# Performance work log

Measured on AMD Instinct MI355X. Metric: run time of the kernel, lower is better.

## Reference

```python
import jax, jax.numpy as jnp
import numpy as np

E, H, I = 8, 1024, 512          # experts, hidden, moe_intermediate
NG, TKG, TOPK = 4, 2, 4          # n_group, topk_group, num_experts_per_tok
SCALE = 2.5                      # routed_scaling_factor


def _mlp(x, wg, wu, wd):
    # SwiGLU MLP: down(silu(gate(x)) * up(x)), all bias-free
    return (jax.nn.silu(x @ wg) * (x @ wu)) @ wd


def setup_inputs() -> dict:
    key = jax.random.key(0)
    ks = jax.random.split(key, 8)
    s = 0.02
    return {
        "hidden_states": jax.random.normal(ks[0], (32, 256, H), jnp.float32),
        "gate_w": jax.random.normal(ks[1], (E, H), jnp.float32) * np.float32(np.sqrt(2.0 / H)),
        "correction_bias": jnp.zeros((E,), jnp.float32),
        "Wg": jax.random.normal(ks[2], (E, H, I), jnp.float32) * s,
        "Wu": jax.random.normal(ks[3], (E, H, I), jnp.float32) * s,
        "Wd": jax.random.normal(ks[4], (E, I, H), jnp.float32) * s,
        "Wg_s": jax.random.normal(ks[5], (H, I), jnp.float32) * s,
        "Wu_s": jax.random.normal(ks[6], (H, I), jnp.float32) * s,
        "Wd_s": jax.random.normal(ks[7], (I, H), jnp.float32) * s,
    }


def reference(hidden_states, gate_w, correction_bias, Wg, Wu, Wd, Wg_s, Wu_s, Wd_s):
    B, T, _ = hidden_states.shape
    x = hidden_states.reshape(-1, H)                     # [N, H]
    N = x.shape[0]

    # ---- TopkRouter + route_tokens_to_experts (float32 router math) ----
    logits = x @ gate_w.T                                # [N, E]
    scores = jax.nn.sigmoid(logits)
    scores_c = scores + correction_bias                  # scores for choice
    grp = scores_c.reshape(N, NG, E // NG)
    group_scores = jnp.sum(jax.lax.top_k(grp, 2)[0], axis=-1)        # [N, NG]
    grp_idx = jax.lax.top_k(group_scores, TKG)[1]                    # [N, TKG]
    group_mask = jnp.zeros_like(group_scores).at[
        jnp.arange(N)[:, None], grp_idx].set(1.0)                    # [N, NG]
    score_mask = jnp.repeat(group_mask, E // NG, axis=-1) > 0.5      # [N, E]
    scores_for_choice = jnp.where(score_mask, scores_c, 0.0)
    topk_idx = jax.lax.top_k(scores_for_choice, TOPK)[1]             # [N, K]
    topk_w = jnp.take_along_axis(scores, topk_idx, axis=-1)          # [N, K]
    topk_w = topk_w / (jnp.sum(topk_w, axis=-1, keepdims=True) + 1e-20)
    topk_w = topk_w * SCALE

    # ---- DSNaiveMoE: equivalent dense-expert combine ----
    # combine weight per (token, expert); zero for unrouted pairs, so the
    # dense evaluation produces exactly the gather/scatter loop's result.
    cw = jnp.sum(jax.nn.one_hot(topk_idx, E, dtype=topk_w.dtype) * topk_w[..., None], axis=1)  # [N, E]
    g = jnp.einsum('nh,ehi->eni', x, Wg)
    u = jnp.einsum('nh,ehi->eni', x, Wu)
    y = jnp.einsum('eni,eih->enh', jax.nn.silu(g) * u, Wd)           # [E, N, H]
    routed = jnp.einsum('enh,ne->nh', y, cw)                          # [N, H]

    # ---- shared expert on residual input (replaces residual add) ----
    out = routed + _mlp(x, Wg_s, Wu_s, Wd_s)
    return out.reshape(B, T, H)
```

## Files before the change

kernel.cpp:

```cpp
#include <hip/hip_runtime.h>

#define E_ 8
#define H_ 1024
#define I_ 512
#define NE 9
#define NTOK 8192

typedef __bf16 bf16;
typedef __bf16 bf16x8 __attribute__((ext_vector_type(8)));
typedef __bf16 bf16x4 __attribute__((ext_vector_type(4)));
typedef float f32x4 __attribute__((ext_vector_type(4)));

__device__ __forceinline__ void gload16(const bf16* g, bf16* l) {
  __builtin_amdgcn_global_load_lds(
      (const __attribute__((address_space(1))) void*)g,
      (__attribute__((address_space(3))) void*)l,
      16, 0, 0);
}

__global__ __launch_bounds__(256) void convert_kernel(
    const float* __restrict__ x, bf16* __restrict__ xb) {
  int i = blockIdx.x * 256 + threadIdx.x;
  f32x4 v = ((const f32x4*)x)[i];
  bf16x4 o = {(bf16)v.x, (bf16)v.y, (bf16)v.z, (bf16)v.w};
  ((bf16x4*)xb)[i] = o;
}

__global__ __launch_bounds__(256) void router_kernel(
    const float* __restrict__ x, const float* __restrict__ gw,
    const float* __restrict__ bias, int4* __restrict__ topk_e,
    float4* __restrict__ topk_w) {
  int t = threadIdx.x;
  int l = t & 63, w = t >> 6;
  int n = blockIdx.x * 4 + w;
  const f32x4* xr = (const f32x4*)(x + (size_t)n * H_ + l * 16);
  float xv[16];
#pragma unroll
  for (int q = 0; q < 4; q++) {
    f32x4 v = xr[q];
    xv[q * 4 + 0] = v.x; xv[q * 4 + 1] = v.y; xv[q * 4 + 2] = v.z; xv[q * 4 + 3] = v.w;
  }
  float s[E_], sc[E_];
#pragma unroll
  for (int e = 0; e < E_; e++) {
    const f32x4* gr = (const f32x4*)(gw + e * H_ + l * 16);
    float acc = 0.f;
#pragma unroll
    for (int q = 0; q < 4; q++) {
      f32x4 g = gr[q];
      acc += xv[q * 4 + 0] * g.x + xv[q * 4 + 1] * g.y + xv[q * 4 + 2] * g.z + xv[q * 4 + 3] * g.w;
    }
#pragma unroll
    for (int off = 32; off > 0; off >>= 1) acc += __shfl_xor(acc, off, 64);
    float sig = 1.f / (1.f + __expf(-acc));
    s[e] = sig;
    sc[e] = sig + bias[e];
  }
  if (l == 0) {
    float gs[4];
#pragma unroll
    for (int g = 0; g < 4; g++) gs[g] = sc[2 * g] + sc[2 * g + 1];
    int g0 = 0;
    for (int g = 1; g < 4; g++) if (gs[g] > gs[g0]) g0 = g;
    int g1 = -1;
    for (int g = 0; g < 4; g++) {
      if (g == g0) continue;
      if (g1 < 0 || gs[g] > gs[g1]) g1 = g;
    }
    int es[4] = {2 * g0, 2 * g0 + 1, 2 * g1, 2 * g1 + 1};
    float wsum = 1e-20f;
    for (int j = 0; j < 4; j++) wsum += s[es[j]];
    float inv = 2.5f / wsum;
    topk_e[n] = (int4){es[0], es[1], es[2], es[3]};
    topk_w[n] = (float4){s[es[0]] * inv, s[es[1]] * inv, s[es[2]] * inv, s[es[3]] * inv};
  }
}

__global__ __launch_bounds__(256) void compact_kernel(
    const int4* __restrict__ topk_e, const float4* __restrict__ topk_w,
    int* __restrict__ cnt, int* __restrict__ idx, float* __restrict__ cwp,
    int* __restrict__ tokpos) {
  __shared__ int hist[E_];
  __shared__ int base[E_];
  int t = threadIdx.x;
  if (t < E_) hist[t] = 0;
  __syncthreads();
  int n = blockIdx.x * 256 + t;
  int4 e4 = topk_e[n];
  float4 w4 = topk_w[n];
  int le[4] = {e4.x, e4.y, e4.z, e4.w};
  float lw[4] = {w4.x, w4.y, w4.z, w4.w};
  int lpos[4];
#pragma unroll
  for (int j = 0; j < 4; j++) lpos[j] = atomicAdd(&hist[le[j]], 1);
  __syncthreads();
  if (t < E_) base[t] = atomicAdd(&cnt[t], hist[t]);
  __syncthreads();
#pragma unroll
  for (int j = 0; j < 4; j++) {
    int p = base[le[j]] + lpos[j];
    idx[le[j] * NTOK + p] = n;
    cwp[le[j] * NTOK + p] = lw[j];
    tokpos[n * 4 + j] = (le[j] << 13) | p;
  }
}

__global__ __launch_bounds__(256) void transpose_kernel(
    const float* __restrict__ Wg, const float* __restrict__ Wu,
    const float* __restrict__ Wd, const float* __restrict__ Wgs,
    const float* __restrict__ Wus, const float* __restrict__ Wds,
    bf16* __restrict__ BgT, bf16* __restrict__ BuT, bf16* __restrict__ WdT) {
  __shared__ bf16 tile[32][33];
  int job = blockIdx.x >> 9;
  int tl = blockIdx.x & 511;
  const float* src;
  bf16* dst;
  int C, dst_ld;
  if (job < 18) {
    int e = job % 9;
    if (job < 9) src = (e < 8) ? Wg + (size_t)e * H_ * I_ : Wgs;
    else         src = (e < 8) ? Wu + (size_t)e * H_ * I_ : Wus;
    dst = ((job < 9) ? BgT : BuT) + (size_t)e * I_ * H_;
    C = I_; dst_ld = H_;
  } else {
    int e = job - 18;
    src = (e < 8) ? Wd + (size_t)e * I_ * H_ : Wds;
    dst = WdT + (size_t)e * H_ * I_;
    C = H_; dst_ld = I_;
  }
  int n_tc = C >> 5;
  int tr = tl / n_tc, tc = tl % n_tc;
  int tx = threadIdx.x & 31, ty = threadIdx.x >> 5;
#pragma unroll
  for (int j = 0; j < 4; j++) {
    int r = tr * 32 + ty + j * 8;
    tile[ty + j * 8][tx] = (bf16)src[(size_t)r * C + tc * 32 + tx];
  }
  __syncthreads();
#pragma unroll
  for (int j = 0; j < 4; j++) {
    int c = tc * 32 + ty + j * 8;
    dst[(size_t)c * dst_ld + tr * 32 + tx] = tile[tx][ty + j * 8];
  }
}


__global__ __launch_bounds__(256, 2) void gemm1_kernel(
    const bf16* __restrict__ X, const bf16* __restrict__ BgT,
    const bf16* __restrict__ BuT, const int* __restrict__ idx,
    const float* __restrict__ cwp, const int* __restrict__ cnt,
    bf16* __restrict__ Tc) {
  int slot = blockIdx.y;
  int e = slot >> 6;
  int m0 = (slot & 63) * 128;
  int ne = (e < 8) ? cnt[e] : NTOK;
  if (m0 >= ne) return;

  __shared__ bf16 As[128 * 64], Bgs[128 * 64], Bus[128 * 64];
  int t = threadIdx.x;
  int l = t & 63, w = t >> 6;
  int wm = w >> 1, wn = w & 1;
  int n0 = blockIdx.x * 128;

  f32x4 accg[4][4], accu[4][4];
#pragma unroll
  for (int mi = 0; mi < 4; mi++)
#pragma unroll
    for (int ni = 0; ni < 4; ni++) {
      accg[mi][ni] = (f32x4){0.f, 0.f, 0.f, 0.f};
      accu[mi][ni] = (f32x4){0.f, 0.f, 0.f, 0.f};
    }

  int srow = t >> 3;
  int scol = (((t & 7) ^ ((t >> 3) & 7)) * 8);
  int rid[4];
#pragma unroll
  for (int i = 0; i < 4; i++) {
    int r = m0 + srow + 32 * i;
    rid[i] = (e < 8) ? ((r < ne) ? idx[e * NTOK + r] : 0) : r;
  }
  const bf16* gg = BgT + (size_t)e * I_ * H_ + (size_t)(n0 + srow) * H_ + scol;
  const bf16* gu = BuT + (size_t)e * I_ * H_ + (size_t)(n0 + srow) * H_ + scol;
  bf16* la = As + w * 512;
  bf16* lg = Bgs + w * 512;
  bf16* lu = Bus + w * 512;

  for (int k0 = 0; k0 < H_; k0 += 64) {
#pragma unroll
    for (int i = 0; i < 4; i++) {
      gload16(X + (size_t)rid[i] * H_ + scol + k0, la + i * 2048);
      gload16(gg + (size_t)i * 32 * H_ + k0, lg + i * 2048);
      gload16(gu + (size_t)i * 32 * H_ + k0, lu + i * 2048);
    }
    __syncthreads();
#pragma unroll
    for (int ks = 0; ks < 2; ks++) {
      int ko = (((ks * 4 + (l >> 4)) ^ (l & 7)) * 8);
      int ar = wm * 64 + (l & 15);
      int br = wn * 64 + (l & 15);
      bf16x8 af[4], bg[4], bu[4];
#pragma unroll
      for (int mi = 0; mi < 4; mi++)
        af[mi] = *(const bf16x8*)(As + (ar + mi * 16) * 64 + ko);
#pragma unroll
      for (int ni = 0; ni < 4; ni++) {
        bg[ni] = *(const bf16x8*)(Bgs + (br + ni * 16) * 64 + ko);
        bu[ni] = *(const bf16x8*)(Bus + (br + ni * 16) * 64 + ko);
      }
#pragma unroll
      for (int mi = 0; mi < 4; mi++)
#pragma unroll
        for (int ni = 0; ni < 4; ni++) {
          accg[mi][ni] = __builtin_amdgcn_mfma_f32_16x16x32_bf16(af[mi], bg[ni], accg[mi][ni], 0, 0, 0);
          accu[mi][ni] = __builtin_amdgcn_mfma_f32_16x16x32_bf16(af[mi], bu[ni], accu[mi][ni], 0, 0, 0);
        }
    }
    __syncthreads();
  }
#pragma unroll
  for (int mi = 0; mi < 4; mi++) {
#pragma unroll
    for (int r = 0; r < 4; r++) {
      int lr = wm * 64 + mi * 16 + (l >> 4) * 4 + r;
      int pr = m0 + lr;
      if (pr < ne) {
        float c = (e < 8) ? cwp[e * NTOK + pr] : 1.0f;
#pragma unroll
        for (int ni = 0; ni < 4; ni++) {
          float g = accg[mi][ni][r];
          float u = accu[mi][ni][r];
          float val = c * (g / (1.f + __expf(-g))) * u;
          int col = n0 + wn * 64 + ni * 16 + (l & 15);
          Tc[((size_t)e * NTOK + pr) * I_ + col] = (bf16)val;
        }
      }
    }
  }
}

__global__ __launch_bounds__(256, 3) void gemm2s_kernel(
    const bf16* __restrict__ Tc, const bf16* __restrict__ WdT,
    float* __restrict__ out) {
  __shared__ bf16 As[128 * 64], Bs[128 * 64];
  int t = threadIdx.x;
  int l = t & 63, w = t >> 6;
  int wm = w >> 1, wn = w & 1;
  int m0 = blockIdx.y * 128;
  int n0 = blockIdx.x * 128;

  f32x4 acc[4][4];
#pragma unroll
  for (int mi = 0; mi < 4; mi++)
#pragma unroll
    for (int ni = 0; ni < 4; ni++) acc[mi][ni] = (f32x4){0.f, 0.f, 0.f, 0.f};

  int srow = t >> 3;
  int scol = (((t & 7) ^ ((t >> 3) & 7)) * 8);
  const bf16* ga = Tc + (size_t)8 * NTOK * I_ + (size_t)(m0 + srow) * I_ + scol;
  const bf16* gb = WdT + (size_t)8 * H_ * I_ + (size_t)(n0 + srow) * I_ + scol;
  bf16* la = As + w * 512;
  bf16* lb = Bs + w * 512;

  for (int k0 = 0; k0 < I_; k0 += 64) {
#pragma unroll
    for (int i = 0; i < 4; i++) {
      gload16(ga + (size_t)i * 32 * I_ + k0, la + i * 2048);
      gload16(gb + (size_t)i * 32 * I_ + k0, lb + i * 2048);
    }
    __syncthreads();
#pragma unroll
    for (int ks = 0; ks < 2; ks++) {
      int ko = (((ks * 4 + (l >> 4)) ^ (l & 7)) * 8);
      int ar = wm * 64 + (l & 15);
      int br = wn * 64 + (l & 15);
      bf16x8 af[4], bfv[4];
#pragma unroll
      for (int mi = 0; mi < 4; mi++)
        af[mi] = *(const bf16x8*)(As + (ar + mi * 16) * 64 + ko);
#pragma unroll
      for (int ni = 0; ni < 4; ni++)
        bfv[ni] = *(const bf16x8*)(Bs + (br + ni * 16) * 64 + ko);
#pragma unroll
      for (int mi = 0; mi < 4; mi++)
#pragma unroll
        for (int ni = 0; ni < 4; ni++)
          acc[mi][ni] = __builtin_amdgcn_mfma_f32_16x16x32_bf16(af[mi], bfv[ni], acc[mi][ni], 0, 0, 0);
    }
    __syncthreads();
  }
#pragma unroll
  for (int mi = 0; mi < 4; mi++) {
#pragma unroll
    for (int r = 0; r < 4; r++) {
      int row = m0 + wm * 64 + mi * 16 + (l >> 4) * 4 + r;
#pragma unroll
      for (int ni = 0; ni < 4; ni++) {
        int col = n0 + wn * 64 + ni * 16 + (l & 15);
        out[(size_t)row * H_ + col] = acc[mi][ni][r];
      }
    }
  }
}

__global__ __launch_bounds__(256, 3) void gemm2r_kernel(
    const bf16* __restrict__ Tc, const bf16* __restrict__ WdT,
    const int* __restrict__ cnt, bf16* __restrict__ Yp) {
  int slot = blockIdx.y;
  int e = slot >> 6;
  int m0 = (slot & 63) * 128;
  int ne = cnt[e];
  if (m0 >= ne) return;
  int off_e = 0;
  for (int ee = 0; ee < e; ee++) off_e += cnt[ee];

  __shared__ bf16 As[128 * 64], Bs[128 * 64];
  int t = threadIdx.x;
  int l = t & 63, w = t >> 6;
  int wm = w >> 1, wn = w & 1;
  int n0 = blockIdx.x * 128;

  f32x4 acc[4][4];
#pragma unroll
  for (int mi = 0; mi < 4; mi++)
#pragma unroll
    for (int ni = 0; ni < 4; ni++) acc[mi][ni] = (f32x4){0.f, 0.f, 0.f, 0.f};

  int srow = t >> 3;
  int scol = (((t & 7) ^ ((t >> 3) & 7)) * 8);
  const bf16* ga = Tc + (size_t)e * NTOK * I_ + (size_t)(m0 + srow) * I_ + scol;
  const bf16* gb = WdT + (size_t)e * H_ * I_ + (size_t)(n0 + srow) * I_ + scol;
  bf16* la = As + w * 512;
  bf16* lb = Bs + w * 512;

  for (int k0 = 0; k0 < I_; k0 += 64) {
#pragma unroll
    for (int i = 0; i < 4; i++) {
      gload16(ga + (size_t)i * 32 * I_ + k0, la + i * 2048);
      gload16(gb + (size_t)i * 32 * I_ + k0, lb + i * 2048);
    }
    __syncthreads();
#pragma unroll
    for (int ks = 0; ks < 2; ks++) {
      int ko = (((ks * 4 + (l >> 4)) ^ (l & 7)) * 8);
      int ar = wm * 64 + (l & 15);
      int br = wn * 64 + (l & 15);
      bf16x8 af[4], bfv[4];
#pragma unroll
      for (int mi = 0; mi < 4; mi++)
        af[mi] = *(const bf16x8*)(As + (ar + mi * 16) * 64 + ko);
#pragma unroll
      for (int ni = 0; ni < 4; ni++)
        bfv[ni] = *(const bf16x8*)(Bs + (br + ni * 16) * 64 + ko);
#pragma unroll
      for (int mi = 0; mi < 4; mi++)
#pragma unroll
        for (int ni = 0; ni < 4; ni++)
          acc[mi][ni] = __builtin_amdgcn_mfma_f32_16x16x32_bf16(af[mi], bfv[ni], acc[mi][ni], 0, 0, 0);
    }
    __syncthreads();
  }
#pragma unroll
  for (int mi = 0; mi < 4; mi++) {
#pragma unroll
    for (int r = 0; r < 4; r++) {
      int lr = wm * 64 + mi * 16 + (l >> 4) * 4 + r;
      int pr = m0 + lr;
      if (pr < ne) {
#pragma unroll
        for (int ni = 0; ni < 4; ni++) {
          int col = n0 + wn * 64 + ni * 16 + (l & 15);
          Yp[(size_t)(off_e + pr) * H_ + col] = (bf16)acc[mi][ni][r];
        }
      }
    }
  }
}

__global__ __launch_bounds__(256) void combine_kernel(
    const int* __restrict__ cnt, const int* __restrict__ tokpos,
    const bf16* __restrict__ Yp, float* __restrict__ out) {
  int t = threadIdx.x;
  int tok = blockIdx.x * 2 + (t >> 7);
  int cb = (t & 127) * 8;
  int off[E_];
  int a = 0;
#pragma unroll
  for (int e = 0; e < E_; e++) { off[e] = a; a += cnt[e]; }
  float* op = out + (size_t)tok * H_ + cb;
  f32x4 o0 = *(const f32x4*)(op);
  f32x4 o1 = *(const f32x4*)(op + 4);
  float sum[8] = {o0.x, o0.y, o0.z, o0.w, o1.x, o1.y, o1.z, o1.w};
#pragma unroll
  for (int j = 0; j < 4; j++) {
    int tp = tokpos[tok * 4 + j];
    int e = tp >> 13, p = tp & 8191;
    bf16x8 v = *(const bf16x8*)(Yp + (size_t)(off[e] + p) * H_ + cb);
#pragma unroll
    for (int q = 0; q < 8; q++) sum[q] += (float)v[q];
  }
  *(f32x4*)(op) = (f32x4){sum[0], sum[1], sum[2], sum[3]};
  *(f32x4*)(op + 4) = (f32x4){sum[4], sum[5], sum[6], sum[7]};
}

extern "C" void kernel_launch(void* const* d_in, const int* in_sizes, int n_in,
                              void* d_out, int out_size, void* d_ws, size_t ws_size,
                              hipStream_t stream) {
  const float* x   = (const float*)d_in[0];
  const float* gw  = (const float*)d_in[1];
  const float* cb  = (const float*)d_in[2];
  const float* Wg  = (const float*)d_in[3];
  const float* Wu  = (const float*)d_in[4];
  const float* Wd  = (const float*)d_in[5];
  const float* Wgs = (const float*)d_in[6];
  const float* Wus = (const float*)d_in[7];
  const float* Wds = (const float*)d_in[8];

  char* ws = (char*)d_ws;
  size_t off = 0;
  int*    cnt    = (int*)(ws + off);    off += 64;
  int*    idx    = (int*)(ws + off);    off += (size_t)E_ * NTOK * 4;
  float*  cwp    = (float*)(ws + off);  off += (size_t)E_ * NTOK * 4;
  int4*   topk_e = (int4*)(ws + off);   off += (size_t)NTOK * 16;
  float4* topk_w = (float4*)(ws + off); off += (size_t)NTOK * 16;
  int*    tokpos = (int*)(ws + off);    off += (size_t)NTOK * 4 * 4;
  bf16* BgT = (bf16*)(ws + off);  off += (size_t)NE * I_ * H_ * 2;
  bf16* BuT = (bf16*)(ws + off);  off += (size_t)NE * I_ * H_ * 2;
  bf16* WdT = (bf16*)(ws + off);  off += (size_t)NE * H_ * I_ * 2;
  bf16* Xb  = (bf16*)(ws + off);  off += (size_t)NTOK * H_ * 2;
  bf16* Tc  = (bf16*)(ws + off);  off += (size_t)NE * NTOK * I_ * 2;
  bf16* Yp  = (bf16*)(ws + off);  off += (size_t)4 * NTOK * H_ * 2;

  hipMemsetAsync(cnt, 0, 64, stream);
  hipLaunchKernelGGL(convert_kernel, dim3(NTOK * H_ / 1024), dim3(256), 0, stream,
                     x, Xb);
  hipLaunchKernelGGL(transpose_kernel, dim3(27 * 512), dim3(256), 0, stream,
                     Wg, Wu, Wd, Wgs, Wus, Wds, BgT, BuT, WdT);
  hipLaunchKernelGGL(router_kernel, dim3(NTOK / 4), dim3(256), 0, stream,
                     x, gw, cb, topk_e, topk_w);
  hipLaunchKernelGGL(compact_kernel, dim3(NTOK / 256), dim3(256), 0, stream,
                     topk_e, topk_w, cnt, idx, cwp, tokpos);
  hipLaunchKernelGGL(gemm1_kernel, dim3(4, NE * 64), dim3(256), 0, stream,
                     Xb, BgT, BuT, idx, cwp, cnt, Tc);
  hipLaunchKernelGGL(gemm2s_kernel, dim3(8, 64), dim3(256), 0, stream,
                     Tc, WdT, (float*)d_out);
  hipLaunchKernelGGL(gemm2r_kernel, dim3(8, E_ * 64), dim3(256), 0, stream,
                     Tc, WdT, cnt, Yp);
  hipLaunchKernelGGL(combine_kernel, dim3(NTOK / 2), dim3(256), 0, stream,
                     cnt, tokpos, Yp, (float*)d_out);
}
```

Before: 387.9 us.

## Fuse prep kernels and pack expert rows into a compact slot grid

Merges the bf16 conversion, weight transpose (now with 64x64 tiles) and router into one prep kernel, removing two launches. The router batches its eight shuffle reductions and computes the sigmoid only on lane 0. Expert rows are packed contiguously, with slots decoded from the counts, so gemm1 and gemm2 launch 328 row tiles instead of 576, most of which used to exit early. The shared expert now goes through the unified gemm2 into bf16 Yp and is summed in combine. That drops a separate kernel and the fp32 read-modify-write of out, at the cost of rounding the shared-expert output to bf16.

Result: faster. 379.4 us (-2.2%).

```diff
diff --git a/kernel.cpp b/kernel.cpp
--- a/kernel.cpp
+++ b/kernel.cpp
@@ -5,6 +5,7 @@
 #define I_ 512
 #define NE 9
 #define NTOK 8192
+#define NROWS 40960
 
 typedef __bf16 bf16;
 typedef __bf16 bf16x8 __attribute__((ext_vector_type(8)));
@@ -18,21 +19,68 @@
       16, 0, 0);
 }
 
-__global__ __launch_bounds__(256) void convert_kernel(
-    const float* __restrict__ x, bf16* __restrict__ xb) {
-  int i = blockIdx.x * 256 + threadIdx.x;
-  f32x4 v = ((const f32x4*)x)[i];
-  bf16x4 o = {(bf16)v.x, (bf16)v.y, (bf16)v.z, (bf16)v.w};
-  ((bf16x4*)xb)[i] = o;
-}
-
-__global__ __launch_bounds__(256) void router_kernel(
+#define PREP_CONV 2048
+#define PREP_TRANS 3456
+__global__ __launch_bounds__(256) void prep_kernel(
     const float* __restrict__ x, const float* __restrict__ gw,
-    const float* __restrict__ bias, int4* __restrict__ topk_e,
-    float4* __restrict__ topk_w) {
+    const float* __restrict__ bias,
+    const float* __restrict__ Wg, const float* __restrict__ Wu,
+    const float* __restrict__ Wd, const float* __restrict__ Wgs,
+    const float* __restrict__ Wus, const float* __restrict__ Wds,
+    bf16* __restrict__ xb, bf16* __restrict__ BgT, bf16* __restrict__ BuT,
+    bf16* __restrict__ WdT, int4* __restrict__ topk_e, float4* __restrict__ topk_w) {
+  __shared__ bf16 tile[64][66];
+  int bid = blockIdx.x;
   int t = threadIdx.x;
+
+  if (bid < PREP_CONV) {
+    size_t base = (size_t)bid * 1024 + t;
+#pragma unroll
+    for (int j = 0; j < 4; j++) {
+      f32x4 v = ((const f32x4*)x)[base + 256 * j];
+      bf16x4 o = {(bf16)v.x, (bf16)v.y, (bf16)v.z, (bf16)v.w};
+      ((bf16x4*)xb)[base + 256 * j] = o;
+    }
+    return;
+  }
+  if (bid < PREP_CONV + PREP_TRANS) {
+    int b = bid - PREP_CONV;
+    int job = b >> 7;
+    int tl = b & 127;
+    const float* src;
+    bf16* dst;
+    int C, dst_ld, tr, tc;
+    if (job < 18) {
+      int e = job % 9;
+      if (job < 9) src = (e < 8) ? Wg + (size_t)e * H_ * I_ : Wgs;
+      else         src = (e < 8) ? Wu + (size_t)e * H_ * I_ : Wus;
+      dst = ((job < 9) ? BgT : BuT) + (size_t)e * I_ * H_;
+      C = I_; dst_ld = H_;
+      tr = tl >> 3; tc = tl & 7;
+    } else {
+      int e = job - 18;
+      src = (e < 8) ? Wd + (size_t)e * I_ * H_ : Wds;
+      dst = WdT + (size_t)e * H_ * I_;
+      C = H_; dst_ld = I_;
+      tr = tl >> 4; tc = tl & 15;
+    }
+    int lx = t & 63, ly = t >> 6;
+#pragma unroll
+    for (int j = 0; j < 16; j++) {
+      int rl = j * 4 + ly;
+      tile[lx][rl] = (bf16)src[(size_t)(tr * 64 + rl) * C + tc * 64 + lx];
+    }
+    __syncthreads();
+#pragma unroll
+    for (int j = 0; j < 16; j++) {
+      int cl = j * 4 + ly;
+      dst[(size_t)(tc * 64 + cl) * dst_ld + tr * 64 + lx] = tile[cl][lx];
+    }
+    return;
+  }
+  int rb = bid - PREP_CONV - PREP_TRANS;
   int l = t & 63, w = t >> 6;
-  int n = blockIdx.x * 4 + w;
+  int n = rb * 4 + w;
   const f32x4* xr = (const f32x4*)(x + (size_t)n * H_ + l * 16);
   float xv[16];
 #pragma unroll
@@ -40,23 +88,33 @@
     f32x4 v = xr[q];
     xv[q * 4 + 0] = v.x; xv[q * 4 + 1] = v.y; xv[q * 4 + 2] = v.z; xv[q * 4 + 3] = v.w;
   }
-  float s[E_], sc[E_];
+  float acc[E_];
 #pragma unroll
   for (int e = 0; e < E_; e++) {
     const f32x4* gr = (const f32x4*)(gw + e * H_ + l * 16);
-    float acc = 0.f;
+    float a = 0.f;
 #pragma unroll
     for (int q = 0; q < 4; q++) {
       f32x4 g = gr[q];
-      acc += xv[q * 4 + 0] * g.x + xv[q * 4 + 1] * g.y + xv[q * 4 + 2] * g.z + xv[q * 4 + 3] * g.w;
-    }
-#pragma unroll
-    for (int off = 32; off > 0; off >>= 1) acc += __shfl_xor(acc, off, 64);
-    float sig = 1.f / (1.f + __expf(-acc));
-    s[e] = sig;
-    sc[e] = sig + bias[e];
+      a += xv[q * 4 + 0] * g.x + xv[q * 4 + 1] * g.y + xv[q * 4 + 2] * g.z + xv[q * 4 + 3] * g.w;
+    }
+    acc[e] = a;
+  }
+#pragma unroll
+  for (int off = 32; off > 0; off >>= 1) {
+    float tmp[E_];
+#pragma unroll
+    for (int e = 0; e < E_; e++) tmp[e] = __shfl_xor(acc[e], off, 64);
+#pragma unroll
+    for (int e = 0; e < E_; e++) acc[e] += tmp[e];
   }
   if (l == 0) {
+    float s[E_], sc[E_];
+#pragma unroll
+    for (int e = 0; e < E_; e++) {
+      s[e] = 1.f / (1.f + __expf(-acc[e]));
+      sc[e] = s[e] + bias[e];
+    }
     float gs[4];
 #pragma unroll
     for (int g = 0; g < 4; g++) gs[g] = sc[2 * g] + sc[2 * g + 1];
@@ -105,43 +163,17 @@
   }
 }
 
-__global__ __launch_bounds__(256) void transpose_kernel(
-    const float* __restrict__ Wg, const float* __restrict__ Wu,
-    const float* __restrict__ Wd, const float* __restrict__ Wgs,
-    const float* __restrict__ Wus, const float* __restrict__ Wds,
-    bf16* __restrict__ BgT, bf16* __restrict__ BuT, bf16* __restrict__ WdT) {
-  __shared__ bf16 tile[32][33];
-  int job = blockIdx.x >> 9;
-  int tl = blockIdx.x & 511;
-  const float* src;
-  bf16* dst;
-  int C, dst_ld;
-  if (job < 18) {
-    int e = job % 9;
-    if (job < 9) src = (e < 8) ? Wg + (size_t)e * H_ * I_ : Wgs;
-    else         src = (e < 8) ? Wu + (size_t)e * H_ * I_ : Wus;
-    dst = ((job < 9) ? BgT : BuT) + (size_t)e * I_ * H_;
-    C = I_; dst_ld = H_;
-  } else {
-    int e = job - 18;
-    src = (e < 8) ? Wd + (size_t)e * I_ * H_ : Wds;
-    dst = WdT + (size_t)e * H_ * I_;
-    C = H_; dst_ld = I_;
-  }
-  int n_tc = C >> 5;
-  int tr = tl / n_tc, tc = tl % n_tc;
-  int tx = threadIdx.x & 31, ty = threadIdx.x >> 5;
-#pragma unroll
-  for (int j = 0; j < 4; j++) {
-    int r = tr * 32 + ty + j * 8;
-    tile[ty + j * 8][tx] = (bf16)src[(size_t)r * C + tc * 32 + tx];
-  }
-  __syncthreads();
-#pragma unroll
-  for (int j = 0; j < 4; j++) {
-    int c = tc * 32 + ty + j * 8;
-    dst[(size_t)c * dst_ld + tr * 32 + tx] = tile[tx][ty + j * 8];
-  }
+__device__ __forceinline__ bool slot_decode(const int* cnt, int slot,
+                                            int& e, int& m0, int& ne, int& off_e) {
+  int off = 0, s = slot;
+  for (int ee = 0; ee < NE; ee++) {
+    int c = (ee < E_) ? cnt[ee] : NTOK;
+    int tl = (c + 127) >> 7;
+    if (s < tl) { e = ee; m0 = s * 128; ne = c; off_e = off; return true; }
+    s -= tl;
+    off += c;
+  }
+  return false;
 }
 
 
@@ -150,11 +182,8 @@
     const bf16* __restrict__ BuT, const int* __restrict__ idx,
     const float* __restrict__ cwp, const int* __restrict__ cnt,
     bf16* __restrict__ Tc) {
-  int slot = blockIdx.y;
-  int e = slot >> 6;
-  int m0 = (slot & 63) * 128;
-  int ne = (e < 8) ? cnt[e] : NTOK;
-  if (m0 >= ne) return;
+  int e, m0, ne, off_e;
+  if (!slot_decode(cnt, blockIdx.y, e, m0, ne, off_e)) return;
 
   __shared__ bf16 As[128 * 64], Bgs[128 * 64], Bus[128 * 64];
   int t = threadIdx.x;
@@ -231,87 +260,18 @@
           float u = accu[mi][ni][r];
           float val = c * (g / (1.f + __expf(-g))) * u;
           int col = n0 + wn * 64 + ni * 16 + (l & 15);
-          Tc[((size_t)e * NTOK + pr) * I_ + col] = (bf16)val;
+          Tc[(size_t)(off_e + pr) * I_ + col] = (bf16)val;
         }
       }
     }
   }
 }
 
-__global__ __launch_bounds__(256, 3) void gemm2s_kernel(
-    const bf16* __restrict__ Tc, const bf16* __restrict__ WdT,
-    float* __restrict__ out) {
-  __shared__ bf16 As[128 * 64], Bs[128 * 64];
-  int t = threadIdx.x;
-  int l = t & 63, w = t >> 6;
-  int wm = w >> 1, wn = w & 1;
-  int m0 = blockIdx.y * 128;
-  int n0 = blockIdx.x * 128;
-
-  f32x4 acc[4][4];
-#pragma unroll
-  for (int mi = 0; mi < 4; mi++)
-#pragma unroll
-    for (int ni = 0; ni < 4; ni++) acc[mi][ni] = (f32x4){0.f, 0.f, 0.f, 0.f};
-
-  int srow = t >> 3;
-  int scol = (((t & 7) ^ ((t >> 3) & 7)) * 8);
-  const bf16* ga = Tc + (size_t)8 * NTOK * I_ + (size_t)(m0 + srow) * I_ + scol;
-  const bf16* gb = WdT + (size_t)8 * H_ * I_ + (size_t)(n0 + srow) * I_ + scol;
-  bf16* la = As + w * 512;
-  bf16* lb = Bs + w * 512;
-
-  for (int k0 = 0; k0 < I_; k0 += 64) {
-#pragma unroll
-    for (int i = 0; i < 4; i++) {
-      gload16(ga + (size_t)i * 32 * I_ + k0, la + i * 2048);
-      gload16(gb + (size_t)i * 32 * I_ + k0, lb + i * 2048);
-    }
-    __syncthreads();
-#pragma unroll
-    for (int ks = 0; ks < 2; ks++) {
-      int ko = (((ks * 4 + (l >> 4)) ^ (l & 7)) * 8);
-      int ar = wm * 64 + (l & 15);
-      int br = wn * 64 + (l & 15);
-      bf16x8 af[4], bfv[4];
-#pragma unroll
-      for (int mi = 0; mi < 4; mi++)
-        af[mi] = *(const bf16x8*)(As + (ar + mi * 16) * 64 + ko);
-#pragma unroll
-      for (int ni = 0; ni < 4; ni++)
-        bfv[ni] = *(const bf16x8*)(Bs + (br + ni * 16) * 64 + ko);
-#pragma unroll
-      for (int mi = 0; mi < 4; mi++)
-#pragma unroll
-        for (int ni = 0; ni < 4; ni++)
-          acc[mi][ni] = __builtin_amdgcn_mfma_f32_16x16x32_bf16(af[mi], bfv[ni], acc[mi][ni], 0, 0, 0);
-    }
-    __syncthreads();
-  }
-#pragma unroll
-  for (int mi = 0; mi < 4; mi++) {
-#pragma unroll
-    for (int r = 0; r < 4; r++) {
-      int row = m0 + wm * 64 + mi * 16 + (l >> 4) * 4 + r;
-#pragma unroll
-      for (int ni = 0; ni < 4; ni++) {
-        int col = n0 + wn * 64 + ni * 16 + (l & 15);
-        out[(size_t)row * H_ + col] = acc[mi][ni][r];
-      }
-    }
-  }
-}
-
-__global__ __launch_bounds__(256, 3) void gemm2r_kernel(
+__global__ __launch_bounds__(256, 3) void gemm2_kernel(
     const bf16* __restrict__ Tc, const bf16* __restrict__ WdT,
     const int* __restrict__ cnt, bf16* __restrict__ Yp) {
-  int slot = blockIdx.y;
-  int e = slot >> 6;
-  int m0 = (slot & 63) * 128;
-  int ne = cnt[e];
-  if (m0 >= ne) return;
-  int off_e = 0;
-  for (int ee = 0; ee < e; ee++) off_e += cnt[ee];
+  int e, m0, ne, off_e;
+  if (!slot_decode(cnt, blockIdx.y, e, m0, ne, off_e)) return;
 
   __shared__ bf16 As[128 * 64], Bs[128 * 64];
   int t = threadIdx.x;
@@ -327,7 +287,7 @@
 
   int srow = t >> 3;
   int scol = (((t & 7) ^ ((t >> 3) & 7)) * 8);
-  const bf16* ga = Tc + (size_t)e * NTOK * I_ + (size_t)(m0 + srow) * I_ + scol;
+  const bf16* ga = Tc + (size_t)(off_e + m0 + srow) * I_ + scol;
   const bf16* gb = WdT + (size_t)e * H_ * I_ + (size_t)(n0 + srow) * I_ + scol;
   bf16* la = As + w * 512;
   bf16* lb = Bs + w * 512;
@@ -386,10 +346,12 @@
   int a = 0;
 #pragma unroll
   for (int e = 0; e < E_; e++) { off[e] = a; a += cnt[e]; }
-  float* op = out + (size_t)tok * H_ + cb;
-  f32x4 o0 = *(const f32x4*)(op);
-  f32x4 o1 = *(const f32x4*)(op + 4);
-  float sum[8] = {o0.x, o0.y, o0.z, o0.w, o1.x, o1.y, o1.z, o1.w};
+  float sum[8];
+  {
+    bf16x8 v = *(const bf16x8*)(Yp + (size_t)(32768 + tok) * H_ + cb);
+#pragma unroll
+    for (int q = 0; q < 8; q++) sum[q] = (float)v[q];
+  }
 #pragma unroll
   for (int j = 0; j < 4; j++) {
     int tp = tokpos[tok * 4 + j];
@@ -398,6 +360,7 @@
 #pragma unroll
     for (int q = 0; q < 8; q++) sum[q] += (float)v[q];
   }
+  float* op = out + (size_t)tok * H_ + cb;
   *(f32x4*)(op) = (f32x4){sum[0], sum[1], sum[2], sum[3]};
   *(f32x4*)(op + 4) = (f32x4){sum[4], sum[5], sum[6], sum[7]};
 }
@@ -427,23 +390,18 @@
   bf16* BuT = (bf16*)(ws + off);  off += (size_t)NE * I_ * H_ * 2;
   bf16* WdT = (bf16*)(ws + off);  off += (size_t)NE * H_ * I_ * 2;
   bf16* Xb  = (bf16*)(ws + off);  off += (size_t)NTOK * H_ * 2;
-  bf16* Tc  = (bf16*)(ws + off);  off += (size_t)NE * NTOK * I_ * 2;
-  bf16* Yp  = (bf16*)(ws + off);  off += (size_t)4 * NTOK * H_ * 2;
+  bf16* Tc  = (bf16*)(ws + off);  off += (size_t)NROWS * I_ * 2;
+  bf16* Yp  = (bf16*)(ws + off);  off += (size_t)NROWS * H_ * 2;
 
   hipMemsetAsync(cnt, 0, 64, stream);
-  hipLaunchKernelGGL(convert_kernel, dim3(NTOK * H_ / 1024), dim3(256), 0, stream,
-                     x, Xb);
-  hipLaunchKernelGGL(transpose_kernel, dim3(27 * 512), dim3(256), 0, stream,
-                     Wg, Wu, Wd, Wgs, Wus, Wds, BgT, BuT, WdT);
-  hipLaunchKernelGGL(router_kernel, dim3(NTOK / 4), dim3(256), 0, stream,
-                     x, gw, cb, topk_e, topk_w);
+  hipLaunchKernelGGL(prep_kernel, dim3(PREP_CONV + PREP_TRANS + NTOK / 4), dim3(256), 0, stream,
+                     x, gw, cb, Wg, Wu, Wd, Wgs, Wus, Wds,
+                     Xb, BgT, BuT, WdT, topk_e, topk_w);
   hipLaunchKernelGGL(compact_kernel, dim3(NTOK / 256), dim3(256), 0, stream,
                      topk_e, topk_w, cnt, idx, cwp, tokpos);
-  hipLaunchKernelGGL(gemm1_kernel, dim3(4, NE * 64), dim3(256), 0, stream,
+  hipLaunchKernelGGL(gemm1_kernel, dim3(4, 328), dim3(256), 0, stream,
                      Xb, BgT, BuT, idx, cwp, cnt, Tc);
-  hipLaunchKernelGGL(gemm2s_kernel, dim3(8, 64), dim3(256), 0, stream,
-                     Tc, WdT, (float*)d_out);
-  hipLaunchKernelGGL(gemm2r_kernel, dim3(8, E_ * 64), dim3(256), 0, stream,
+  hipLaunchKernelGGL(gemm2_kernel, dim3(8, 328), dim3(256), 0, stream,
                      Tc, WdT, cnt, Yp);
   hipLaunchKernelGGL(combine_kernel, dim3(NTOK / 2), dim3(256), 0, stream,
                      cnt, tokpos, Yp, (float*)d_out);
```
